# Kernel tuning notes

Measured on AMD Instinct MI355X. Metric: run time of the kernel, lower is better.

The kernel has to match this reference:

```python
import jax, jax.numpy as jnp
import numpy as np

B, L, G, H = 16384, 4096, 30000, 256
LN_EPS = 1e-5


def setup_inputs() -> dict:
    key = jax.random.key(0)
    k0, k1, k2, k3 = jax.random.split(key, 4)
    x = jax.random.uniform(k0, (B, L), dtype=jnp.float32)          # cell x gene expression
    gene_idx = jax.random.randint(k1, (L,), 0, G)                   # irregular gene indices
    emb = jax.random.normal(k2, (G, H), dtype=jnp.float32) * 0.005  # gene embedding table
    W1 = jax.random.normal(k3, (H, H), dtype=jnp.float32) * (1.0 / np.sqrt(H))
    b1 = jnp.zeros((H,), dtype=jnp.float32)
    gamma = jnp.ones((H,), dtype=jnp.float32)
    beta = jnp.zeros((H,), dtype=jnp.float32)
    return {"x": x, "emb": emb, "W1": W1, "b1": b1, "gamma": gamma,
            "beta": beta, "gene_idx": gene_idx}


def reference(x, emb, W1, b1, gamma, beta, gene_idx):
    # OmicsEmbedder: gather gene embeddings, then weighted aggregation per cell
    feat = emb[gene_idx]                     # [L, H]  F.embedding gather
    h = x @ feat                             # [B, H]  torch.sparse.mm(x, feat)
    # extra_linear: Linear -> ReLU -> Dropout(eval: identity) -> LayerNorm
    h = jax.nn.relu(h @ W1 + b1)             # [B, H]
    mu = jnp.mean(h, axis=-1, keepdims=True)
    var = jnp.mean(jnp.square(h - mu), axis=-1, keepdims=True)
    return gamma * (h - mu) * jax.lax.rsqrt(var + LN_EPS) + beta
```

## Files before the change

kernel.cpp:

```cpp
#include <hip/hip_runtime.h>
#include <stdint.h>

#define B_DIM 16384
#define L_DIM 4096
#define H_DIM 256
#define LN_EPS 1e-5f
#define PERM4(r) ((((r) & 7) << 1) | (((r) >> 3) & 1))

typedef unsigned short u16;
typedef __attribute__((ext_vector_type(4))) float f32x4;
typedef __attribute__((ext_vector_type(8))) short short8;

__device__ __forceinline__ u16 f2bf(float f) {
  union { float f; uint32_t u; } v; v.f = f;
  uint32_t u = v.u;
  u += 0x7FFFu + ((u >> 16) & 1u);
  return (u16)(u >> 16);
}

__device__ __forceinline__ short8 cvt8(const float4& u, const float4& v) {
  short8 o;
  o[0] = (short)f2bf(u.x); o[1] = (short)f2bf(u.y);
  o[2] = (short)f2bf(u.z); o[3] = (short)f2bf(u.w);
  o[4] = (short)f2bf(v.x); o[5] = (short)f2bf(v.y);
  o[6] = (short)f2bf(v.z); o[7] = (short)f2bf(v.w);
  return o;
}

__device__ __forceinline__ void gload_lds16(const void* g, void* l) {
  __builtin_amdgcn_global_load_lds((const __attribute__((address_space(1))) void*)g,
                                   (__attribute__((address_space(3))) void*)l, 16, 0, 0);
}

__global__ __launch_bounds__(256) void prep_frag(const float* __restrict__ src,
                                                 const int* __restrict__ idx,
                                                 u16* __restrict__ dst) {
  const int t = threadIdx.x;
  const int l = t & 63;
  const int w = t >> 6;
  const int frag = blockIdx.x * 4 + w;
  const int kstep = frag >> 4;
  const int nt = frag & 15;
  const int n = nt * 16 + (l & 15);
  const int kbase = kstep * 32 + (l >> 4) * 8;
  short8 v;
#pragma unroll
  for (int j = 0; j < 8; ++j) {
    const int k = kbase + j;
    const int g = idx ? idx[k] : k;
    v[j] = (short)f2bf(src[(size_t)g * H_DIM + n]);
  }
  *reinterpret_cast<short8*>(dst + ((size_t)frag * 64 + l) * 8) = v;
}

__global__ __launch_bounds__(256, 2) void fused(const float* __restrict__ x,
                                                const u16* __restrict__ fragB,
                                                const u16* __restrict__ fragW,
                                                const float* __restrict__ b1,
                                                const float* __restrict__ gmm,
                                                const float* __restrict__ bta,
                                                float* __restrict__ out) {
  __shared__ __align__(16) char pool[81920];
  const int t = threadIdx.x;
  const int l = t & 63;
  const int wv = t >> 6;
  const int m0 = blockIdx.x * 32;
  const float* xbase = x + (size_t)m0 * L_DIM;
  char* const Ab = pool + 65536;

  f32x4 acc[2][4] = {};
  short8 bP[8], bQ[8];

#pragma unroll
  for (int i = 0; i < 2; ++i) {
    const int R = (wv * 2 + i) * 4 + (l >> 4);
    const int c16 = (l & 15) ^ PERM4(R);
    gload_lds16(xbase + (size_t)R * L_DIM + c16 * 4, Ab + (wv * 2 + i) * 1024);
  }
#pragma unroll
  for (int f = 0; f < 8; ++f) {
    const int frag = (f >> 2) * 16 + wv * 4 + (f & 3);
    bP[f] = *(const short8*)(fragB + (size_t)frag * 512 + l * 8);
  }

  auto stage = [&](int S, short8 (&cur)[8], short8 (&nxt)[8]) {
    asm volatile("s_waitcnt vmcnt(0)" ::: "memory");
    __builtin_amdgcn_s_barrier();
    __builtin_amdgcn_sched_barrier(0);
    if (S < 63) {
#pragma unroll
      for (int i = 0; i < 2; ++i) {
        const int R = (wv * 2 + i) * 4 + (l >> 4);
        const int c16 = (l & 15) ^ PERM4(R);
        gload_lds16(xbase + (size_t)R * L_DIM + (S + 1) * 64 + c16 * 4,
                    Ab + ((S + 1) & 1) * 8192 + (wv * 2 + i) * 1024);
      }
#pragma unroll
      for (int f = 0; f < 8; ++f) {
        const int frag = (2 * (S + 1) + (f >> 2)) * 16 + wv * 4 + (f & 3);
        nxt[f] = *(const short8*)(fragB + (size_t)frag * 512 + l * 8);
      }
    }
    __builtin_amdgcn_sched_barrier(0);
    const char* bA = Ab + (S & 1) * 8192;
#pragma unroll
    for (int ks = 0; ks < 2; ++ks) {
      short8 af[2];
#pragma unroll
      for (int mi = 0; mi < 2; ++mi) {
        const int row = mi * 16 + (l & 15);
        const int p4 = PERM4(row);
        const int gs = ks * 8 + (l >> 4) * 2;
        const float4 a0 = *(const float4*)(bA + row * 256 + ((gs ^ p4) * 16));
        const float4 a1 = *(const float4*)(bA + row * 256 + (((gs + 1) ^ p4) * 16));
        af[mi] = cvt8(a0, a1);
      }
#pragma unroll
      for (int ntl = 0; ntl < 4; ++ntl)
#pragma unroll
        for (int mi = 0; mi < 2; ++mi)
          acc[mi][ntl] = __builtin_amdgcn_mfma_f32_16x16x32_bf16(
              af[mi], cur[ks * 4 + ntl], acc[mi][ntl], 0, 0, 0);
    }
    asm volatile("s_waitcnt lgkmcnt(0)" ::: "memory");
    __builtin_amdgcn_s_barrier();
  };

  for (int sp = 0; sp < 32; ++sp) {
    stage(sp * 2,     bP, bQ);
    stage(sp * 2 + 1, bQ, bP);
  }

#pragma unroll
  for (int i = 0; i < 4; ++i) {
    const int j = wv * 4 + i;
    gload_lds16(fragW + (size_t)j * 512 + l * 8, pool + 16384 + j * 1024);
  }
#pragma unroll
  for (int mi = 0; mi < 2; ++mi)
#pragma unroll
    for (int rr = 0; rr < 4; ++rr) {
      const int row = mi * 16 + (l >> 4) * 4 + rr;
#pragma unroll
      for (int ntl = 0; ntl < 4; ++ntl) {
        const int col = wv * 64 + ntl * 16 + (l & 15);
        const int ls = (col >> 3) ^ (row & 15);
        *(u16*)(pool + row * 512 + ls * 16 + (col & 7) * 2) = f2bf(acc[mi][ntl][rr]);
      }
    }
  asm volatile("s_waitcnt lgkmcnt(0)" ::: "memory");
  __builtin_amdgcn_s_barrier();

  f32x4 acc2[2][4] = {};
  for (int kt = 0; kt < 8; ++kt) {
    asm volatile("s_waitcnt vmcnt(0)" ::: "memory");
    __builtin_amdgcn_s_barrier();
    __builtin_amdgcn_sched_barrier(0);
    if (kt < 7) {
      const u16* srcW = fragW + (size_t)(kt + 1) * 16 * 512;
      char* dstW = pool + 16384 + ((kt + 1) & 1) * 16384;
#pragma unroll
      for (int i = 0; i < 4; ++i) {
        const int j = wv * 4 + i;
        gload_lds16(srcW + (size_t)j * 512 + l * 8, dstW + j * 1024);
      }
    }
    __builtin_amdgcn_sched_barrier(0);
    const char* bW = pool + 16384 + (kt & 1) * 16384;
    short8 af[2];
#pragma unroll
    for (int mi = 0; mi < 2; ++mi) {
      const int row = mi * 16 + (l & 15);
      af[mi] = *(const short8*)(pool + row * 512 +
                                (((kt * 4 + (l >> 4)) ^ (row & 15)) << 4));
    }
#pragma unroll
    for (int ntl = 0; ntl < 4; ++ntl) {
      const short8 bfv = *(const short8*)(bW + (wv * 4 + ntl) * 1024 + l * 16);
#pragma unroll
      for (int mi = 0; mi < 2; ++mi)
        acc2[mi][ntl] = __builtin_amdgcn_mfma_f32_16x16x32_bf16(af[mi], bfv, acc2[mi][ntl], 0, 0, 0);
    }
    asm volatile("s_waitcnt lgkmcnt(0)" ::: "memory");
    __builtin_amdgcn_s_barrier();
  }

  float bv[4], gg[4], bb[4];
#pragma unroll
  for (int ntl = 0; ntl < 4; ++ntl) {
    const int col = wv * 64 + ntl * 16 + (l & 15);
    bv[ntl] = b1[col]; gg[ntl] = gmm[col]; bb[ntl] = bta[col];
  }
  float* lnred = (float*)(pool + 49152);
#pragma unroll
  for (int mi = 0; mi < 2; ++mi)
#pragma unroll
    for (int rr = 0; rr < 4; ++rr) {
      float s = 0.f, q = 0.f;
#pragma unroll
      for (int ntl = 0; ntl < 4; ++ntl) {
        const float v = fmaxf(acc2[mi][ntl][rr] + bv[ntl], 0.f);
        acc2[mi][ntl][rr] = v; s += v; q += v * v;
      }
#pragma unroll
      for (int m = 1; m < 16; m <<= 1) { s += __shfl_xor(s, m); q += __shfl_xor(q, m); }
      if ((l & 15) == 0) {
        const int row = mi * 16 + (l >> 4) * 4 + rr;
        lnred[(wv * 32 + row) * 2 + 0] = s;
        lnred[(wv * 32 + row) * 2 + 1] = q;
      }
    }
  __syncthreads();
#pragma unroll
  for (int mi = 0; mi < 2; ++mi)
#pragma unroll
    for (int rr = 0; rr < 4; ++rr) {
      const int row = mi * 16 + (l >> 4) * 4 + rr;
      float S = 0.f, Q = 0.f;
#pragma unroll
      for (int w2 = 0; w2 < 4; ++w2) {
        S += lnred[(w2 * 32 + row) * 2 + 0];
        Q += lnred[(w2 * 32 + row) * 2 + 1];
      }
      const float mu = S * (1.0f / 256.0f);
      const float rstd = rsqrtf(Q * (1.0f / 256.0f) - mu * mu + LN_EPS);
      float* op = out + (size_t)(m0 + row) * H_DIM;
#pragma unroll
      for (int ntl = 0; ntl < 4; ++ntl) {
        const int col = wv * 64 + ntl * 16 + (l & 15);
        op[col] = gg[ntl] * (acc2[mi][ntl][rr] - mu) * rstd + bb[ntl];
      }
    }
}

extern "C" void kernel_launch(void* const* d_in, const int* in_sizes, int n_in,
                              void* d_out, int out_size, void* d_ws, size_t ws_size,
                              hipStream_t stream) {
  const float* x    = (const float*)d_in[0];
  const float* emb  = (const float*)d_in[1];
  const float* W1   = (const float*)d_in[2];
  const float* b1   = (const float*)d_in[3];
  const float* gmm  = (const float*)d_in[4];
  const float* bta  = (const float*)d_in[5];
  const int*   gidx = (const int*)d_in[6];
  float* out = (float*)d_out;

  char* ws = (char*)d_ws;
  u16* fragB = (u16*)ws;
  u16* fragW = (u16*)(ws + (size_t)H_DIM * L_DIM * 2);

  prep_frag<<<512, 256, 0, stream>>>(emb, gidx, fragB);
  prep_frag<<<32, 256, 0, stream>>>(W1, nullptr, fragW);
  fused<<<512, 256, 0, stream>>>(x, fragB, fragW, b1, gmm, bta, out);
}
```

Measured before the change: 106.1 us.

## Replace double-buffered K loop with 4-stage LDS pipeline for A and B

Restructures the main GEMM K loop from a 2-stage scheme (A via LDS double buffer, B fragments held in registers) into a 4-deep ring buffer in LDS. Both x tiles and pre-packed embedding fragments are loaded with direct global-to-LDS copies, three stages in flight, and a partial vmcnt wait gates each step. The K step shrinks from 64 to 32, doubling the iteration count but removing the B register prefetch arrays and the trailing barrier per stage. The goal is to hide global memory latency with deeper prefetch and lower register pressure. The cost is more barriers per unit of K and more LDS use.

Measured after the change: 147.1 us. 1.39x slower.

```diff
diff --git a/kernel.cpp b/kernel.cpp
--- a/kernel.cpp
+++ b/kernel.cpp
@@ -5,7 +5,6 @@
 #define L_DIM 4096
 #define H_DIM 256
 #define LN_EPS 1e-5f
-#define PERM4(r) ((((r) & 7) << 1) | (((r) >> 3) & 1))
 
 typedef unsigned short u16;
 typedef __attribute__((ext_vector_type(4))) float f32x4;
@@ -65,71 +64,78 @@
   const int l = t & 63;
   const int wv = t >> 6;
   const int m0 = blockIdx.x * 32;
-  const float* xbase = x + (size_t)m0 * L_DIM;
-  char* const Ab = pool + 65536;
+
+  const int R = wv * 8 + (l >> 3);
+  const int c = (l & 7) ^ (R & 7);
+  const float* asrc = x + (size_t)(m0 + R) * L_DIM + c * 4;
 
   f32x4 acc[2][4] = {};
-  short8 bP[8], bQ[8];
-
-#pragma unroll
-  for (int i = 0; i < 2; ++i) {
-    const int R = (wv * 2 + i) * 4 + (l >> 4);
-    const int c16 = (l & 15) ^ PERM4(R);
-    gload_lds16(xbase + (size_t)R * L_DIM + c16 * 4, Ab + (wv * 2 + i) * 1024);
-  }
-#pragma unroll
-  for (int f = 0; f < 8; ++f) {
-    const int frag = (f >> 2) * 16 + wv * 4 + (f & 3);
-    bP[f] = *(const short8*)(fragB + (size_t)frag * 512 + l * 8);
-  }
-
-  auto stage = [&](int S, short8 (&cur)[8], short8 (&nxt)[8]) {
-    asm volatile("s_waitcnt vmcnt(0)" ::: "memory");
+
+#pragma unroll
+  for (int hn = 0; hn < 3; ++hn) {
+#pragma unroll
+    for (int i = 0; i < 4; ++i) {
+      const int fr = wv * 4 + i;
+      gload_lds16(fragB + ((size_t)(hn * 16 + fr)) * 512 + l * 8,
+                  pool + hn * 16384 + fr * 1024);
+    }
+    gload_lds16(asrc + hn * 32, pool + 65536 + hn * 4096 + wv * 1024);
+    __builtin_amdgcn_sched_barrier(0);
+  }
+
+  auto issue = [&](int hn) {
+    char* Bd = pool + (hn & 3) * 16384;
+#pragma unroll
+    for (int i = 0; i < 4; ++i) {
+      const int fr = wv * 4 + i;
+      gload_lds16(fragB + ((size_t)(hn * 16 + fr)) * 512 + l * 8, Bd + fr * 1024);
+    }
+    gload_lds16(asrc + hn * 32, pool + 65536 + (hn & 3) * 4096 + wv * 1024);
+  };
+
+  auto compute = [&](int h) {
+    const char* Ab = pool + 65536 + (h & 3) * 4096;
+    const char* Bb = pool + (h & 3) * 16384;
+    short8 af[2];
+#pragma unroll
+    for (int mi = 0; mi < 2; ++mi) {
+      const int row = mi * 16 + (l & 15);
+      const int c0 = (l >> 4) * 2;
+      const float4 a0 = *(const float4*)(Ab + row * 128 + ((c0 ^ (row & 7)) * 16));
+      const float4 a1 = *(const float4*)(Ab + row * 128 + (((c0 + 1) ^ (row & 7)) * 16));
+      af[mi] = cvt8(a0, a1);
+    }
+#pragma unroll
+    for (int ni = 0; ni < 4; ++ni) {
+      const short8 bf = *(const short8*)(Bb + (wv * 4 + ni) * 1024 + l * 16);
+#pragma unroll
+      for (int mi = 0; mi < 2; ++mi)
+        acc[mi][ni] = __builtin_amdgcn_mfma_f32_16x16x32_bf16(af[mi], bf, acc[mi][ni], 0, 0, 0);
+    }
+    asm volatile("s_waitcnt lgkmcnt(0)" ::: "memory");
+    __builtin_amdgcn_sched_barrier(0);
+  };
+
+  for (int h = 0; h < 125; ++h) {
+    asm volatile("s_waitcnt vmcnt(10)" ::: "memory");
     __builtin_amdgcn_s_barrier();
     __builtin_amdgcn_sched_barrier(0);
-    if (S < 63) {
-#pragma unroll
-      for (int i = 0; i < 2; ++i) {
-        const int R = (wv * 2 + i) * 4 + (l >> 4);
-        const int c16 = (l & 15) ^ PERM4(R);
-        gload_lds16(xbase + (size_t)R * L_DIM + (S + 1) * 64 + c16 * 4,
-                    Ab + ((S + 1) & 1) * 8192 + (wv * 2 + i) * 1024);
-      }
-#pragma unroll
-      for (int f = 0; f < 8; ++f) {
-        const int frag = (2 * (S + 1) + (f >> 2)) * 16 + wv * 4 + (f & 3);
-        nxt[f] = *(const short8*)(fragB + (size_t)frag * 512 + l * 8);
-      }
-    }
-    __builtin_amdgcn_sched_barrier(0);
-    const char* bA = Ab + (S & 1) * 8192;
-#pragma unroll
-    for (int ks = 0; ks < 2; ++ks) {
-      short8 af[2];
-#pragma unroll
-      for (int mi = 0; mi < 2; ++mi) {
-        const int row = mi * 16 + (l & 15);
-        const int p4 = PERM4(row);
-        const int gs = ks * 8 + (l >> 4) * 2;
-        const float4 a0 = *(const float4*)(bA + row * 256 + ((gs ^ p4) * 16));
-        const float4 a1 = *(const float4*)(bA + row * 256 + (((gs + 1) ^ p4) * 16));
-        af[mi] = cvt8(a0, a1);
-      }
-#pragma unroll
-      for (int ntl = 0; ntl < 4; ++ntl)
-#pragma unroll
-        for (int mi = 0; mi < 2; ++mi)
-          acc[mi][ntl] = __builtin_amdgcn_mfma_f32_16x16x32_bf16(
-              af[mi], cur[ks * 4 + ntl], acc[mi][ntl], 0, 0, 0);
-    }
-    asm volatile("s_waitcnt lgkmcnt(0)" ::: "memory");
-    __builtin_amdgcn_s_barrier();
-  };
-
-  for (int sp = 0; sp < 32; ++sp) {
-    stage(sp * 2,     bP, bQ);
-    stage(sp * 2 + 1, bQ, bP);
-  }
+    issue(h + 3);
+    __builtin_amdgcn_sched_barrier(0);
+    compute(h);
+  }
+  asm volatile("s_waitcnt vmcnt(10)" ::: "memory");
+  __builtin_amdgcn_s_barrier();
+  __builtin_amdgcn_sched_barrier(0);
+  compute(125);
+  asm volatile("s_waitcnt vmcnt(5)" ::: "memory");
+  __builtin_amdgcn_s_barrier();
+  __builtin_amdgcn_sched_barrier(0);
+  compute(126);
+  asm volatile("s_waitcnt vmcnt(0)" ::: "memory");
+  __builtin_amdgcn_s_barrier();
+  __builtin_amdgcn_sched_barrier(0);
+  compute(127);
 
 #pragma unroll
   for (int i = 0; i < 4; ++i) {
```
